# Kernel tuning notes

Hardware: AMD Instinct MI355X
Metric: run time of the kernel (lower is better)

Reference implementation:

```python
import jax, jax.numpy as jnp
import numpy as np

B, S, I, H = 64, 2048, 64, 128


def setup_inputs() -> dict:
    key = jax.random.key(0)
    ks = jax.random.split(key, 4)
    return {
        'x': jax.random.normal(ks[0], (B, S, I), dtype=jnp.float32),
        'w0': jax.random.normal(ks[1], (I, H), dtype=jnp.float32) * 0.1,
        'u0': jax.random.normal(ks[2], (H, H), dtype=jnp.float32) * 0.1,
        'bg0': jnp.ones((1, H), jnp.float32),
        'bu0': jnp.ones((1, H), jnp.float32),
        'zeta0': jnp.full((1, 1), 1.0, jnp.float32),
        'nu0': jnp.full((1, 1), -4.0, jnp.float32),
        'lambd0': jnp.zeros((1,), jnp.float32),
        'gamma0': jnp.full((1,), 0.999, jnp.float32),
        'w1': jax.random.normal(jax.random.fold_in(key, 10), (H, H), dtype=jnp.float32) * 0.1,
        'u1': jax.random.normal(ks[3], (H, H), dtype=jnp.float32) * 0.1,
        'bg1': jnp.ones((1, H), jnp.float32),
        'bu1': jnp.ones((1, H), jnp.float32),
        'zeta1': jnp.full((1, 1), 1.0, jnp.float32),
        'nu1': jnp.full((1, 1), -4.0, jnp.float32),
        'lambd1': jnp.zeros((1,), jnp.float32),
        'gamma1': jnp.full((1,), 0.999, jnp.float32),
    }


def _layer(x_seq, w, u, bg, bu, zeta, nu, lambd, gamma):
    # x_seq: [B, S, in]; precompute input projection for all timesteps
    wx = jnp.einsum('bsi,ih->bsh', x_seq, w)  # [B, S, H]
    sz = jax.nn.sigmoid(zeta)  # [1,1]
    sn = jax.nn.sigmoid(nu)    # [1,1]
    gc = jnp.clip(gamma, 0.0, 1.0)  # [1]
    h0 = jnp.zeros((x_seq.shape[0], u.shape[0]), x_seq.dtype)

    def step(h, wx_t):
        pre = wx_t + h @ u            # [B, H]
        z = jax.nn.sigmoid(pre + bg)  # gate
        h_hat = jnp.tanh(pre + bu)    # update
        h_new = z * h + (sz * (1.0 - z) + sn) * h_hat
        h_comfi = gc * h_new + (1.0 - gc) * lambd
        return h_comfi, h_comfi

    h_T, outs = jax.lax.scan(step, h0, jnp.swapaxes(wx, 0, 1))  # outs: [S, B, H]
    return jnp.swapaxes(outs, 0, 1), h_T


def reference(x, w0, u0, bg0, bu0, zeta0, nu0, lambd0, gamma0,
              w1, u1, bg1, bu1, zeta1, nu1, lambd1, gamma1):
    out0, h0T = _layer(x, w0, u0, bg0, bu0, zeta0, nu0, lambd0, gamma0)
    out1, h1T = _layer(out0, w1, u1, bg1, bu1, zeta1, nu1, lambd1, gamma1)
    h_n = jnp.stack([h0T, h1T], axis=0)  # [num_layers, B, H]
    return out1, h_n
```

## Files before the change

### kernel.cpp

```cpp
#include <hip/hip_runtime.h>
#include <hip/hip_bf16.h>

#define BB 64
#define SS 2048
#define II 64
#define HH 128
#define CH 64

typedef _Float16 half8 __attribute__((ext_vector_type(8)));
typedef float f32x4 __attribute__((ext_vector_type(4)));

#define LOG2E 1.44269504088896340736f

__device__ __forceinline__ float sigm(float x) { return 1.0f / (1.0f + __expf(-x)); }

__global__ __launch_bounds__(256, 4)
void wx0_kernel(const float* __restrict__ x, const float* __restrict__ w0,
                float* __restrict__ wx0) {
  __shared__ float xs[32][64];
  const int tid = threadIdx.x;
  const int j = tid & (HH - 1);
  const int rh = tid >> 7;
  const long row0 = (long)blockIdx.x * 32;

  float w0c[II];
#pragma unroll
  for (int i = 0; i < II; ++i) w0c[i] = w0[i * HH + j];

  const float4* xg = (const float4*)(x + row0 * II);
  float4* xsv = (float4*)&xs[0][0];
  xsv[tid] = xg[tid];
  xsv[tid + 256] = xg[tid + 256];
  __syncthreads();

#pragma unroll
  for (int rp = 0; rp < 16; ++rp) {
    int r = rp * 2 + rh;
    float acc = 0.f;
#pragma unroll
    for (int i = 0; i < II; i += 4) {
      float4 xv = *(const float4*)&xs[r][i];
      acc += w0c[i] * xv.x + w0c[i + 1] * xv.y + w0c[i + 2] * xv.z +
             w0c[i + 3] * xv.w;
    }
    wx0[(row0 + r) * HH + j] = acc;
  }
}

__global__ __launch_bounds__(512, 1)
void scan_kernel(const float* __restrict__ wx0,
                 const float* __restrict__ u0, const float* __restrict__ bg0,
                 const float* __restrict__ bu0, const float* __restrict__ zeta0,
                 const float* __restrict__ nu0, const float* __restrict__ lambd0,
                 const float* __restrict__ gamma0,
                 const float* __restrict__ w1, const float* __restrict__ u1,
                 const float* __restrict__ bg1, const float* __restrict__ bu1,
                 const float* __restrict__ zeta1, const float* __restrict__ nu1,
                 const float* __restrict__ lambd1, const float* __restrict__ gamma1,
                 float* __restrict__ out1, float* __restrict__ hn) {
  const int b = blockIdx.x;
  const int tid = threadIdx.x;
  const int w = tid >> 6;
  const int l = tid & 63;
  const int g = l >> 4;
  const int n = l & 15;
  const int c = 16 * w + n;

  half8 wfA[4], wfB[4], wfC[4];
#pragma unroll
  for (int kt = 0; kt < 4; ++kt) {
    half8 fa, fb, fc;
#pragma unroll
    for (int i = 0; i < 8; ++i) {
      int k = 32 * kt + (i < 4 ? 4 * g + i : 16 + 4 * g + (i - 4));
      fa[i] = (_Float16)u0[k * HH + c];
      fb[i] = (_Float16)w1[k * HH + c];
      fc[i] = (_Float16)u1[k * HH + c];
    }
    wfA[kt] = fa; wfB[kt] = fb; wfC[kt] = fc;
  }

  const float sz0 = sigm(zeta0[0]), sn0 = sigm(nu0[0]);
  const float gc0 = fminf(fmaxf(gamma0[0], 0.f), 1.f);
  const float kc0 = (1.f - gc0) * lambd0[0];
  const float sz1 = sigm(zeta1[0]), sn1 = sigm(nu1[0]);
  const float gc1 = fminf(fmaxf(gamma1[0], 0.f), 1.f);
  const float kc1 = (1.f - gc1) * lambd1[0];
  const float ebg0 = -LOG2E * bg0[c];
  const float ebu0 = -2.f * LOG2E * bu0[c];
  const float ebg1 = -LOG2E * bg1[c];
  const float ebu1 = -2.f * LOG2E * bu1[c];

  auto gate = [](float pre, float hp, float eg, float eu, float sz, float sn,
                 float gc, float kc) -> float {
    float p  = __builtin_amdgcn_exp2f(__builtin_fmaf(pre, -LOG2E, eg));
    float qq = __builtin_amdgcn_exp2f(__builtin_fmaf(pre, -2.f * LOG2E, eu));
    float opp = 1.f + p, opq = 1.f + qq, omq = 1.f - qq;
    float t1 = __builtin_fmaf(sn, opp, sz * p);
    float num = __builtin_fmaf(hp, opq, t1 * omq);
    float hnew = num * __builtin_amdgcn_rcpf(opp * opq);
    return __builtin_fmaf(gc, hnew, kc);
  };

  __shared__ __align__(16) _Float16 Hpk[2][2][160];
  __shared__ __align__(16) float wxb[CH * HH];

  const float* wxg = wx0 + (size_t)b * SS * HH;
  float* outg = out1 + (size_t)b * SS * HH;

  const int wkt = c >> 5;
  const int wr_ = c & 31;
  const int widx = (wkt * 4 + ((wr_ & 15) >> 2)) * 8 + ((wr_ >> 4) << 2) + (wr_ & 3);
  const int rbase = 8 * g;

  {
    const float4* src = (const float4*)(wxg + HH);
    float4* dst = (float4*)wxb;
#pragma unroll
    for (int i = 0; i < 4; ++i) dst[i * 512 + tid] = src[i * 512 + tid];
  }
  float hp0, hp1 = 0.f;
  {
    float h00 = gate(wxg[c], 0.f, ebg0, ebu0, sz0, sn0, gc0, kc0);
    hp0 = h00;
    if (g == 0) {
      Hpk[0][0][widx] = (_Float16)h00;
      Hpk[0][1][widx] = (_Float16)0.f;
    }
  }
  asm volatile("s_waitcnt lgkmcnt(0)" ::: "memory");
  __builtin_amdgcn_s_barrier();

  const f32x4 zero = {0.f, 0.f, 0.f, 0.f};

  half8 a0[4], a1[4];
#pragma unroll
  for (int kt = 0; kt < 4; ++kt) {
    a0[kt] = (half8)(_Float16)0.f;
    a1[kt] = (half8)(_Float16)0.f;
  }

  for (int t = 0; t < SS; ++t) {
    const int rd = t & 1, wb = rd ^ 1;
    const int q = t & (CH - 1);

    if (n == 0) {
#pragma unroll
      for (int kt = 0; kt < 4; ++kt) {
        a0[kt] = __builtin_bit_cast(half8,
                   *(const uint4*)&Hpk[rd][0][kt * 32 + rbase]);
        a1[kt] = __builtin_bit_cast(half8,
                   *(const uint4*)&Hpk[rd][1][kt * 32 + rbase]);
      }
    }
    float wxv = wxb[q * HH + c];

    f32x4 accA, accB, accC;
#pragma unroll
    for (int kt = 0; kt < 4; ++kt) {
      accA = __builtin_amdgcn_mfma_f32_16x16x32_f16(a0[kt], wfA[kt], kt ? accA : zero, 0, 0, 0);
      accB = __builtin_amdgcn_mfma_f32_16x16x32_f16(a0[kt], wfB[kt], kt ? accB : zero, 0, 0, 0);
      accC = __builtin_amdgcn_mfma_f32_16x16x32_f16(a1[kt], wfC[kt], kt ? accC : zero, 0, 0, 0);
    }

    float pre0 = accA[0] + wxv;
    float hc0 = gate(pre0, hp0, ebg0, ebu0, sz0, sn0, gc0, kc0);
    hp0 = hc0;
    if (g == 0) Hpk[wb][0][widx] = (_Float16)hc0;

    float pre1 = accB[0] + accC[0];
    float hc1 = gate(pre1, hp1, ebg1, ebu1, sz1, sn1, gc1, kc1);
    hp1 = hc1;
    if (g == 0) {
      Hpk[wb][1][widx] = (_Float16)hc1;
      outg[(size_t)t * HH + c] = hc1;
      if (t == SS - 2) hn[b * HH + c] = hc0;
      if (t == SS - 1) hn[BB * HH + b * HH + c] = hc1;
    }

    asm volatile("s_waitcnt lgkmcnt(0)" ::: "memory");
    __builtin_amdgcn_s_barrier();

    if (q == CH - 1 && t + 1 < SS) {
      float4* wdst = (float4*)wxb;
#pragma unroll
      for (int i = 0; i < 4; ++i) {
        int flat4 = i * 512 + tid;
        int row = t + 2 + (flat4 >> 5);
        row = row < SS ? row : SS - 1;
        int col4 = flat4 & 31;
        wdst[flat4] = *(const float4*)(wxg + (size_t)row * HH + col4 * 4);
      }
      asm volatile("s_waitcnt lgkmcnt(0)" ::: "memory");
      __builtin_amdgcn_s_barrier();
    }
  }
}

extern "C" void kernel_launch(void* const* d_in, const int* in_sizes, int n_in,
                              void* d_out, int out_size, void* d_ws, size_t ws_size,
                              hipStream_t stream) {
  const float* x      = (const float*)d_in[0];
  const float* w0     = (const float*)d_in[1];
  const float* u0     = (const float*)d_in[2];
  const float* bg0    = (const float*)d_in[3];
  const float* bu0    = (const float*)d_in[4];
  const float* zeta0  = (const float*)d_in[5];
  const float* nu0    = (const float*)d_in[6];
  const float* lambd0 = (const float*)d_in[7];
  const float* gamma0 = (const float*)d_in[8];
  const float* w1     = (const float*)d_in[9];
  const float* u1     = (const float*)d_in[10];
  const float* bg1    = (const float*)d_in[11];
  const float* bu1    = (const float*)d_in[12];
  const float* zeta1  = (const float*)d_in[13];
  const float* nu1    = (const float*)d_in[14];
  const float* lambd1 = (const float*)d_in[15];
  const float* gamma1 = (const float*)d_in[16];

  float* out = (float*)d_out;
  float* hn  = out + (size_t)BB * SS * HH;
  float* wx0 = (float*)d_ws;

  wx0_kernel<<<(BB * SS) / 32, 256, 0, stream>>>(x, w0, wx0);
  scan_kernel<<<BB, 512, 0, stream>>>(wx0, u0, bg0, bu0, zeta0, nu0, lambd0,
                                      gamma0, w1, u1, bg1, bu1, zeta1, nu1,
                                      lambd1, gamma1, out, hn);
}
```

Measured before the change: 887.4 us.

## Pack two batch sequences per scan workgroup and reorder layer MFMA/gate work

Each 1024-thread workgroup of the scan kernel now runs two independent batch rows, each with its own shared-memory state buffers, so the grid shrinks from 64 to 32 workgroups. The MFMA chains and gate evaluation are reordered so layer 1 is computed before layer 0 within each step. The intent is to overlap two sequences' latency-bound recurrences on one CU and shorten the dependency chain. The cost is that the per-step barriers now synchronize both sequences together, only 32 CUs are used, and register pressure per thread rises under the 1024-thread launch bound.

Measured after the change: 1.438 ms. 62.1% more time.

```diff
diff --git a/kernel.cpp b/kernel.cpp
--- a/kernel.cpp
+++ b/kernel.cpp
@@ -6,6 +6,7 @@
 #define II 64
 #define HH 128
 #define CH 64
+#define BPB 2
 
 typedef _Float16 half8 __attribute__((ext_vector_type(8)));
 typedef float f32x4 __attribute__((ext_vector_type(4)));
@@ -47,7 +48,7 @@
   }
 }
 
-__global__ __launch_bounds__(512, 1)
+__global__ __launch_bounds__(1024, 4)
 void scan_kernel(const float* __restrict__ wx0,
                  const float* __restrict__ u0, const float* __restrict__ bg0,
                  const float* __restrict__ bu0, const float* __restrict__ zeta0,
@@ -58,9 +59,11 @@
                  const float* __restrict__ zeta1, const float* __restrict__ nu1,
                  const float* __restrict__ lambd1, const float* __restrict__ gamma1,
                  float* __restrict__ out1, float* __restrict__ hn) {
-  const int b = blockIdx.x;
   const int tid = threadIdx.x;
-  const int w = tid >> 6;
+  const int grp = tid >> 9;
+  const int tl = tid & 511;
+  const int b = blockIdx.x * BPB + grp;
+  const int w = tl >> 6;
   const int l = tid & 63;
   const int g = l >> 4;
   const int n = l & 15;
@@ -102,8 +105,8 @@
     return __builtin_fmaf(gc, hnew, kc);
   };
 
-  __shared__ __align__(16) _Float16 Hpk[2][2][160];
-  __shared__ __align__(16) float wxb[CH * HH];
+  __shared__ __align__(16) _Float16 Hpk[BPB][2][2][160];
+  __shared__ __align__(16) float wxb[BPB][CH * HH];
 
   const float* wxg = wx0 + (size_t)b * SS * HH;
   float* outg = out1 + (size_t)b * SS * HH;
@@ -115,17 +118,17 @@
 
   {
     const float4* src = (const float4*)(wxg + HH);
-    float4* dst = (float4*)wxb;
-#pragma unroll
-    for (int i = 0; i < 4; ++i) dst[i * 512 + tid] = src[i * 512 + tid];
+    float4* dst = (float4*)&wxb[grp][0];
+#pragma unroll
+    for (int i = 0; i < 4; ++i) dst[i * 512 + tl] = src[i * 512 + tl];
   }
   float hp0, hp1 = 0.f;
   {
     float h00 = gate(wxg[c], 0.f, ebg0, ebu0, sz0, sn0, gc0, kc0);
     hp0 = h00;
     if (g == 0) {
-      Hpk[0][0][widx] = (_Float16)h00;
-      Hpk[0][1][widx] = (_Float16)0.f;
+      Hpk[grp][0][0][widx] = (_Float16)h00;
+      Hpk[grp][0][1][widx] = (_Float16)0.f;
     }
   }
   asm volatile("s_waitcnt lgkmcnt(0)" ::: "memory");
@@ -147,45 +150,47 @@
     if (n == 0) {
 #pragma unroll
       for (int kt = 0; kt < 4; ++kt) {
+        a1[kt] = __builtin_bit_cast(half8,
+                   *(const uint4*)&Hpk[grp][rd][1][kt * 32 + rbase]);
         a0[kt] = __builtin_bit_cast(half8,
-                   *(const uint4*)&Hpk[rd][0][kt * 32 + rbase]);
-        a1[kt] = __builtin_bit_cast(half8,
-                   *(const uint4*)&Hpk[rd][1][kt * 32 + rbase]);
+                   *(const uint4*)&Hpk[grp][rd][0][kt * 32 + rbase]);
       }
     }
-    float wxv = wxb[q * HH + c];
+    float wxv = wxb[grp][q * HH + c];
 
     f32x4 accA, accB, accC;
 #pragma unroll
     for (int kt = 0; kt < 4; ++kt) {
+      accC = __builtin_amdgcn_mfma_f32_16x16x32_f16(a1[kt], wfC[kt], kt ? accC : zero, 0, 0, 0);
+      accB = __builtin_amdgcn_mfma_f32_16x16x32_f16(a0[kt], wfB[kt], kt ? accB : zero, 0, 0, 0);
       accA = __builtin_amdgcn_mfma_f32_16x16x32_f16(a0[kt], wfA[kt], kt ? accA : zero, 0, 0, 0);
-      accB = __builtin_amdgcn_mfma_f32_16x16x32_f16(a0[kt], wfB[kt], kt ? accB : zero, 0, 0, 0);
-      accC = __builtin_amdgcn_mfma_f32_16x16x32_f16(a1[kt], wfC[kt], kt ? accC : zero, 0, 0, 0);
-    }
-
-    float pre0 = accA[0] + wxv;
-    float hc0 = gate(pre0, hp0, ebg0, ebu0, sz0, sn0, gc0, kc0);
-    hp0 = hc0;
-    if (g == 0) Hpk[wb][0][widx] = (_Float16)hc0;
+    }
 
     float pre1 = accB[0] + accC[0];
     float hc1 = gate(pre1, hp1, ebg1, ebu1, sz1, sn1, gc1, kc1);
     hp1 = hc1;
     if (g == 0) {
-      Hpk[wb][1][widx] = (_Float16)hc1;
+      Hpk[grp][wb][1][widx] = (_Float16)hc1;
       outg[(size_t)t * HH + c] = hc1;
+      if (t == SS - 1) hn[BB * HH + b * HH + c] = hc1;
+    }
+
+    float pre0 = accA[0] + wxv;
+    float hc0 = gate(pre0, hp0, ebg0, ebu0, sz0, sn0, gc0, kc0);
+    hp0 = hc0;
+    if (g == 0) {
+      Hpk[grp][wb][0][widx] = (_Float16)hc0;
       if (t == SS - 2) hn[b * HH + c] = hc0;
-      if (t == SS - 1) hn[BB * HH + b * HH + c] = hc1;
     }
 
     asm volatile("s_waitcnt lgkmcnt(0)" ::: "memory");
     __builtin_amdgcn_s_barrier();
 
     if (q == CH - 1 && t + 1 < SS) {
-      float4* wdst = (float4*)wxb;
+      float4* wdst = (float4*)&wxb[grp][0];
 #pragma unroll
       for (int i = 0; i < 4; ++i) {
-        int flat4 = i * 512 + tid;
+        int flat4 = i * 512 + tl;
         int row = t + 2 + (flat4 >> 5);
         row = row < SS ? row : SS - 1;
         int col4 = flat4 & 31;
@@ -223,7 +228,8 @@
   float* wx0 = (float*)d_ws;
 
   wx0_kernel<<<(BB * SS) / 32, 256, 0, stream>>>(x, w0, wx0);
-  scan_kernel<<<BB, 512, 0, stream>>>(wx0, u0, bg0, bu0, zeta0, nu0, lambd0,
-                                      gamma0, w1, u1, bg1, bu1, zeta1, nu1,
-                                      lambd1, gamma1, out, hn);
+  scan_kernel<<<BB / BPB, 512 * BPB, 0, stream>>>(wx0, u0, bg0, bu0, zeta0, nu0,
+                                                  lambd0, gamma0, w1, u1, bg1,
+                                                  bu1, zeta1, nu1, lambd1,
+                                                  gamma1, out, hn);
 }
```

## Split layer gates across lane groups and prefetch wx chunks into registers

Applied to the files above, without the earlier changes.

The scan loop now loads hidden-state fragments into four A-matrix rows instead of one. Each lane group therefore gets a valid MFMA result: group 0 computes the layer-0 gate and groups 1–3 compute the layer-1 gate. This replaces every lane evaluating both gates, which halves the transcendental work on the serial recurrence path. The next wx chunk is loaded into registers at the start of each 64-step chunk and written to LDS at its end, which removes the exposed global-load latency and the extra barrier. Output stores move to group 2 and are delayed by one step so they stay off the critical path, at the cost of more registers and some per-lane select logic.

Result: slower. 919.9 us (+3.7%).

```diff
diff --git a/kernel.cpp b/kernel.cpp
--- a/kernel.cpp
+++ b/kernel.cpp
@@ -65,6 +65,7 @@
   const int g = l >> 4;
   const int n = l & 15;
   const int c = 16 * w + n;
+  const bool L0 = (g == 0);
 
   half8 wfA[4], wfB[4], wfC[4];
 #pragma unroll
@@ -80,16 +81,13 @@
     wfA[kt] = fa; wfB[kt] = fb; wfC[kt] = fc;
   }
 
-  const float sz0 = sigm(zeta0[0]), sn0 = sigm(nu0[0]);
-  const float gc0 = fminf(fmaxf(gamma0[0], 0.f), 1.f);
-  const float kc0 = (1.f - gc0) * lambd0[0];
-  const float sz1 = sigm(zeta1[0]), sn1 = sigm(nu1[0]);
-  const float gc1 = fminf(fmaxf(gamma1[0], 0.f), 1.f);
-  const float kc1 = (1.f - gc1) * lambd1[0];
-  const float ebg0 = -LOG2E * bg0[c];
-  const float ebu0 = -2.f * LOG2E * bu0[c];
-  const float ebg1 = -LOG2E * bg1[c];
-  const float ebu1 = -2.f * LOG2E * bu1[c];
+  const float szd = L0 ? sigm(zeta0[0]) : sigm(zeta1[0]);
+  const float snd = L0 ? sigm(nu0[0]) : sigm(nu1[0]);
+  const float gcr = L0 ? gamma0[0] : gamma1[0];
+  const float gcd = fminf(fmaxf(gcr, 0.f), 1.f);
+  const float kcd = (1.f - gcd) * (L0 ? lambd0[0] : lambd1[0]);
+  const float ebgd = -LOG2E * (L0 ? bg0[c] : bg1[c]);
+  const float ebud = -2.f * LOG2E * (L0 ? bu0[c] : bu1[c]);
 
   auto gate = [](float pre, float hp, float eg, float eu, float sz, float sn,
                  float gc, float kc) -> float {
@@ -119,10 +117,14 @@
 #pragma unroll
     for (int i = 0; i < 4; ++i) dst[i * 512 + tid] = src[i * 512 + tid];
   }
-  float hp0, hp1 = 0.f;
+  float hp;
   {
-    float h00 = gate(wxg[c], 0.f, ebg0, ebu0, sz0, sn0, gc0, kc0);
-    hp0 = h00;
+    const float sz0 = sigm(zeta0[0]), sn0 = sigm(nu0[0]);
+    const float gc0 = fminf(fmaxf(gamma0[0], 0.f), 1.f);
+    const float kc0 = (1.f - gc0) * lambd0[0];
+    float h00 = gate(wxg[c], 0.f, -LOG2E * bg0[c], -2.f * LOG2E * bu0[c],
+                     sz0, sn0, gc0, kc0);
+    hp = L0 ? h00 : 0.f;
     if (g == 0) {
       Hpk[0][0][widx] = (_Float16)h00;
       Hpk[0][1][widx] = (_Float16)0.f;
@@ -140,11 +142,17 @@
     a1[kt] = (half8)(_Float16)0.f;
   }
 
+  float4 pf0, pf1, pf2, pf3;
+  float store_val = 0.f;
+  int store_t = -1;
+
   for (int t = 0; t < SS; ++t) {
     const int rd = t & 1, wb = rd ^ 1;
     const int q = t & (CH - 1);
 
-    if (n == 0) {
+    if (store_t >= 0 && g == 2) outg[(size_t)store_t * HH + c] = store_val;
+
+    if ((n & 3) == 0) {
 #pragma unroll
       for (int kt = 0; kt < 4; ++kt) {
         a0[kt] = __builtin_bit_cast(half8,
@@ -155,46 +163,55 @@
     }
     float wxv = wxb[q * HH + c];
 
+    if (q == 0 && t + 1 < SS) {
+      const int flat0 = tid;
+#pragma unroll
+      for (int i = 0; i < 4; ++i) {
+        int flat4 = i * 512 + flat0;
+        int row = t + 65 + (flat4 >> 5);
+        row = row < SS ? row : SS - 1;
+        int col4 = flat4 & 31;
+        float4 v = *(const float4*)(wxg + (size_t)row * HH + col4 * 4);
+        if (i == 0) pf0 = v; else if (i == 1) pf1 = v;
+        else if (i == 2) pf2 = v; else pf3 = v;
+      }
+    }
+
     f32x4 accA, accB, accC;
 #pragma unroll
     for (int kt = 0; kt < 4; ++kt) {
       accA = __builtin_amdgcn_mfma_f32_16x16x32_f16(a0[kt], wfA[kt], kt ? accA : zero, 0, 0, 0);
+      accC = __builtin_amdgcn_mfma_f32_16x16x32_f16(a1[kt], wfC[kt], kt ? accC : zero, 0, 0, 0);
       accB = __builtin_amdgcn_mfma_f32_16x16x32_f16(a0[kt], wfB[kt], kt ? accB : zero, 0, 0, 0);
-      accC = __builtin_amdgcn_mfma_f32_16x16x32_f16(a1[kt], wfC[kt], kt ? accC : zero, 0, 0, 0);
-    }
-
-    float pre0 = accA[0] + wxv;
-    float hc0 = gate(pre0, hp0, ebg0, ebu0, sz0, sn0, gc0, kc0);
-    hp0 = hc0;
-    if (g == 0) Hpk[wb][0][widx] = (_Float16)hc0;
-
-    float pre1 = accB[0] + accC[0];
-    float hc1 = gate(pre1, hp1, ebg1, ebu1, sz1, sn1, gc1, kc1);
-    hp1 = hc1;
+    }
+
+    float pre = L0 ? (accA[0] + wxv) : (accB[0] + accC[0]);
+    float hc = gate(pre, hp, ebgd, ebud, szd, snd, gcd, kcd);
+    hp = hc;
+
     if (g == 0) {
-      Hpk[wb][1][widx] = (_Float16)hc1;
-      outg[(size_t)t * HH + c] = hc1;
-      if (t == SS - 2) hn[b * HH + c] = hc0;
-      if (t == SS - 1) hn[BB * HH + b * HH + c] = hc1;
+      Hpk[wb][0][widx] = (_Float16)hc;
+      if (t == SS - 2) hn[b * HH + c] = hc;
+    }
+    if (g == 1) {
+      Hpk[wb][1][widx] = (_Float16)hc;
+      if (t == SS - 1) hn[BB * HH + b * HH + c] = hc;
+    }
+    if (g == 2) { store_val = hc; store_t = t; }
+
+    if (q == CH - 1 && t + 1 < SS) {
+      float4* wdst = (float4*)wxb;
+      wdst[0 * 512 + tid] = pf0;
+      wdst[1 * 512 + tid] = pf1;
+      wdst[2 * 512 + tid] = pf2;
+      wdst[3 * 512 + tid] = pf3;
     }
 
     asm volatile("s_waitcnt lgkmcnt(0)" ::: "memory");
     __builtin_amdgcn_s_barrier();
-
-    if (q == CH - 1 && t + 1 < SS) {
-      float4* wdst = (float4*)wxb;
-#pragma unroll
-      for (int i = 0; i < 4; ++i) {
-        int flat4 = i * 512 + tid;
-        int row = t + 2 + (flat4 >> 5);
-        row = row < SS ? row : SS - 1;
-        int col4 = flat4 & 31;
-        wdst[flat4] = *(const float4*)(wxg + (size_t)row * HH + col4 * 4);
-      }
-      asm volatile("s_waitcnt lgkmcnt(0)" ::: "memory");
-      __builtin_amdgcn_s_barrier();
-    }
-  }
+  }
+
+  if (store_t >= 0 && g == 2) outg[(size_t)store_t * HH + c] = store_val;
 }
 
 extern "C" void kernel_launch(void* const* d_in, const int* in_sizes, int n_in,
```

## Split scan waves into per-layer roles with two column tiles each

Applied to the files above, without the earlier changes.

Waves 0-3 now compute only the layer-0 recurrence and waves 4-7 only layer 1. Each wave covers 32 hidden columns with two 16-column MFMA tiles instead of 16 columns across both layers. The aim is to halve the per-thread gate math and the register weight fragments, so the two layers run in parallel wave groups. The cost is that layer-1 waves now issue 16 MFMAs per step instead of 12, which may lengthen the per-step critical path, and the two groups do unequal work.

Measured after the change: 1.090 ms. +22.9%, slower.

```diff
diff --git a/kernel.cpp b/kernel.cpp
--- a/kernel.cpp
+++ b/kernel.cpp
@@ -61,35 +61,41 @@
   const int b = blockIdx.x;
   const int tid = threadIdx.x;
   const int w = tid >> 6;
+  const int wq = w & 3;
+  const bool role = (w >= 4);
   const int l = tid & 63;
   const int g = l >> 4;
   const int n = l & 15;
-  const int c = 16 * w + n;
-
-  half8 wfA[4], wfB[4], wfC[4];
-#pragma unroll
-  for (int kt = 0; kt < 4; ++kt) {
-    half8 fa, fb, fc;
-#pragma unroll
-    for (int i = 0; i < 8; ++i) {
-      int k = 32 * kt + (i < 4 ? 4 * g + i : 16 + 4 * g + (i - 4));
-      fa[i] = (_Float16)u0[k * HH + c];
-      fb[i] = (_Float16)w1[k * HH + c];
-      fc[i] = (_Float16)u1[k * HH + c];
-    }
-    wfA[kt] = fa; wfB[kt] = fb; wfC[kt] = fc;
-  }
-
-  const float sz0 = sigm(zeta0[0]), sn0 = sigm(nu0[0]);
-  const float gc0 = fminf(fmaxf(gamma0[0], 0.f), 1.f);
-  const float kc0 = (1.f - gc0) * lambd0[0];
-  const float sz1 = sigm(zeta1[0]), sn1 = sigm(nu1[0]);
-  const float gc1 = fminf(fmaxf(gamma1[0], 0.f), 1.f);
-  const float kc1 = (1.f - gc1) * lambd1[0];
-  const float ebg0 = -LOG2E * bg0[c];
-  const float ebu0 = -2.f * LOG2E * bu0[c];
-  const float ebg1 = -LOG2E * bg1[c];
-  const float ebu1 = -2.f * LOG2E * bu1[c];
+  const int cd = 32 * wq + ((g & 1) << 4) + n;
+
+  half8 wfP[2][4], wfQ[2][4];
+  {
+    const float* WP = role ? w1 : u0;
+#pragma unroll
+    for (int nt = 0; nt < 2; ++nt) {
+      const int col = 32 * wq + 16 * nt + n;
+#pragma unroll
+      for (int kt = 0; kt < 4; ++kt) {
+        half8 fp, fq;
+#pragma unroll
+        for (int i = 0; i < 8; ++i) {
+          int k = 32 * kt + (i < 4 ? 4 * g + i : 16 + 4 * g + (i - 4));
+          fp[i] = (_Float16)WP[k * HH + col];
+          fq[i] = role ? (_Float16)u1[k * HH + col] : (_Float16)0.f;
+        }
+        wfP[nt][kt] = fp;
+        wfQ[nt][kt] = fq;
+      }
+    }
+  }
+
+  const float szd = role ? sigm(zeta1[0]) : sigm(zeta0[0]);
+  const float snd = role ? sigm(nu1[0]) : sigm(nu0[0]);
+  const float gcr = role ? gamma1[0] : gamma0[0];
+  const float gcd = fminf(fmaxf(gcr, 0.f), 1.f);
+  const float kcd = (1.f - gcd) * (role ? lambd1[0] : lambd0[0]);
+  const float ebgd = -LOG2E * (role ? bg1[cd] : bg0[cd]);
+  const float ebud = -2.f * LOG2E * (role ? bu1[cd] : bu0[cd]);
 
   auto gate = [](float pre, float hp, float eg, float eu, float sz, float sn,
                  float gc, float kc) -> float {
@@ -108,10 +114,11 @@
   const float* wxg = wx0 + (size_t)b * SS * HH;
   float* outg = out1 + (size_t)b * SS * HH;
 
-  const int wkt = c >> 5;
-  const int wr_ = c & 31;
+  const int wkt = cd >> 5;
+  const int wr_ = cd & 31;
   const int widx = (wkt * 4 + ((wr_ & 15) >> 2)) * 8 + ((wr_ >> 4) << 2) + (wr_ & 3);
   const int rbase = 8 * g;
+  const bool writer = (g < 2);
 
   {
     const float4* src = (const float4*)(wxg + HH);
@@ -119,63 +126,82 @@
 #pragma unroll
     for (int i = 0; i < 4; ++i) dst[i * 512 + tid] = src[i * 512 + tid];
   }
-  float hp0, hp1 = 0.f;
+  float hp;
   {
-    float h00 = gate(wxg[c], 0.f, ebg0, ebu0, sz0, sn0, gc0, kc0);
-    hp0 = h00;
-    if (g == 0) {
-      Hpk[0][0][widx] = (_Float16)h00;
-      Hpk[0][1][widx] = (_Float16)0.f;
-    }
+    const float sz0 = sigm(zeta0[0]), sn0 = sigm(nu0[0]);
+    const float gc0 = fminf(fmaxf(gamma0[0], 0.f), 1.f);
+    const float kc0 = (1.f - gc0) * lambd0[0];
+    float h00 = gate(wxg[cd], 0.f, -LOG2E * bg0[cd], -2.f * LOG2E * bu0[cd],
+                     sz0, sn0, gc0, kc0);
+    hp = role ? 0.f : h00;
+    if (!role && writer) Hpk[0][0][widx] = (_Float16)h00;
+    if (role && writer)  Hpk[0][1][widx] = (_Float16)0.f;
   }
   asm volatile("s_waitcnt lgkmcnt(0)" ::: "memory");
   __builtin_amdgcn_s_barrier();
 
   const f32x4 zero = {0.f, 0.f, 0.f, 0.f};
 
-  half8 a0[4], a1[4];
+  half8 ha[4], hb[4];
 #pragma unroll
   for (int kt = 0; kt < 4; ++kt) {
-    a0[kt] = (half8)(_Float16)0.f;
-    a1[kt] = (half8)(_Float16)0.f;
+    ha[kt] = (half8)(_Float16)0.f;
+    hb[kt] = (half8)(_Float16)0.f;
   }
 
   for (int t = 0; t < SS; ++t) {
     const int rd = t & 1, wb = rd ^ 1;
     const int q = t & (CH - 1);
 
-    if (n == 0) {
+    if ((n & 3) == 0) {
+#pragma unroll
+      for (int kt = 0; kt < 4; ++kt)
+        ha[kt] = __builtin_bit_cast(half8,
+                   *(const uint4*)&Hpk[rd][0][kt * 32 + rbase]);
+      if (role) {
+#pragma unroll
+        for (int kt = 0; kt < 4; ++kt)
+          hb[kt] = __builtin_bit_cast(half8,
+                     *(const uint4*)&Hpk[rd][1][kt * 32 + rbase]);
+      }
+    }
+
+    float pre;
+    if (!role) {
+      float wxv = wxb[q * HH + cd];
+      f32x4 acc0, acc1;
 #pragma unroll
       for (int kt = 0; kt < 4; ++kt) {
-        a0[kt] = __builtin_bit_cast(half8,
-                   *(const uint4*)&Hpk[rd][0][kt * 32 + rbase]);
-        a1[kt] = __builtin_bit_cast(half8,
-                   *(const uint4*)&Hpk[rd][1][kt * 32 + rbase]);
-      }
-    }
-    float wxv = wxb[q * HH + c];
-
-    f32x4 accA, accB, accC;
-#pragma unroll
-    for (int kt = 0; kt < 4; ++kt) {
-      accA = __builtin_amdgcn_mfma_f32_16x16x32_f16(a0[kt], wfA[kt], kt ? accA : zero, 0, 0, 0);
-      accB = __builtin_amdgcn_mfma_f32_16x16x32_f16(a0[kt], wfB[kt], kt ? accB : zero, 0, 0, 0);
-      accC = __builtin_amdgcn_mfma_f32_16x16x32_f16(a1[kt], wfC[kt], kt ? accC : zero, 0, 0, 0);
-    }
-
-    float pre0 = accA[0] + wxv;
-    float hc0 = gate(pre0, hp0, ebg0, ebu0, sz0, sn0, gc0, kc0);
-    hp0 = hc0;
-    if (g == 0) Hpk[wb][0][widx] = (_Float16)hc0;
-
-    float pre1 = accB[0] + accC[0];
-    float hc1 = gate(pre1, hp1, ebg1, ebu1, sz1, sn1, gc1, kc1);
-    hp1 = hc1;
-    if (g == 0) {
-      Hpk[wb][1][widx] = (_Float16)hc1;
-      outg[(size_t)t * HH + c] = hc1;
-      if (t == SS - 2) hn[b * HH + c] = hc0;
-      if (t == SS - 1) hn[BB * HH + b * HH + c] = hc1;
+        acc0 = __builtin_amdgcn_mfma_f32_16x16x32_f16(ha[kt], wfP[0][kt], kt ? acc0 : zero, 0, 0, 0);
+        acc1 = __builtin_amdgcn_mfma_f32_16x16x32_f16(ha[kt], wfP[1][kt], kt ? acc1 : zero, 0, 0, 0);
+      }
+      pre = ((g & 1) ? acc1[0] : acc0[0]) + wxv;
+    } else {
+      f32x4 accB0, accB1, accC0, accC1;
+#pragma unroll
+      for (int kt = 0; kt < 4; ++kt) {
+        accB0 = __builtin_amdgcn_mfma_f32_16x16x32_f16(ha[kt], wfP[0][kt], kt ? accB0 : zero, 0, 0, 0);
+        accC0 = __builtin_amdgcn_mfma_f32_16x16x32_f16(hb[kt], wfQ[0][kt], kt ? accC0 : zero, 0, 0, 0);
+        accB1 = __builtin_amdgcn_mfma_f32_16x16x32_f16(ha[kt], wfP[1][kt], kt ? accB1 : zero, 0, 0, 0);
+        accC1 = __builtin_amdgcn_mfma_f32_16x16x32_f16(hb[kt], wfQ[1][kt], kt ? accC1 : zero, 0, 0, 0);
+      }
+      pre = (g & 1) ? (accB1[0] + accC1[0]) : (accB0[0] + accC0[0]);
+    }
+
+    float hc = gate(pre, hp, ebgd, ebud, szd, snd, gcd, kcd);
+    hp = hc;
+
+    if (!role) {
+      if (writer) {
+        Hpk[wb][0][widx] = (_Float16)hc;
+        if (t == SS - 2) hn[b * HH + cd] = hc;
+      }
+    } else {
+      if (writer) {
+        Hpk[wb][1][widx] = (_Float16)hc;
+        outg[(size_t)t * HH + cd] = hc;
+        if (t == SS - 1) hn[BB * HH + b * HH + cd] = hc;
+      }
     }
 
     asm volatile("s_waitcnt lgkmcnt(0)" ::: "memory");
```
